# Kernel optimization log

Measured on AMD Instinct MI355X. Metric: run time of the kernel, lower is better.

## Reference

```python
import jax, jax.numpy as jnp
import numpy as np

BETA = 0.25  # cfg.vq_commitment


def setup_inputs() -> dict:
    key = jax.random.key(0)
    k1, k2 = jax.random.split(key)
    residual = jax.random.normal(k1, (16, 2048, 512), dtype=jnp.float32)
    emb_weight = jax.random.normal(k2, (1024, 512), dtype=jnp.float32) * 0.02
    return {"residual": residual, "emb_weight": emb_weight}


def reference(residual, emb_weight):
    # Euclidean branch (vq_cosine=False), no factorized projection (rvq_code_dim<=0)
    r = residual                                     # [B, T, D]
    z2 = jnp.sum(r * r, axis=-1, keepdims=True)      # [B, T, 1]
    e2 = jnp.sum(emb_weight * emb_weight, axis=-1)   # [N]
    # dist[b,t,n] = ||r_bt||^2 + ||e_n||^2 - 2 <r_bt, e_n>
    dist = z2 + e2 - 2.0 * jnp.einsum('btd,nd->btn', r, emb_weight)
    idx = jnp.argmin(dist, axis=-1)                  # [B, T] int
    z_q = emb_weight[idx]                            # gather, [B, T, D]
    # straight-through estimator
    z_st = residual + jax.lax.stop_gradient(z_q - residual)
    commit = jnp.mean((jax.lax.stop_gradient(z_q) - residual) ** 2)
    codebook = jnp.mean((z_q - jax.lax.stop_gradient(residual)) ** 2)
    loss = BETA * commit + codebook
    return (z_st, loss, dist, idx)
```

## Files before the change

### kernel.cpp

```cpp
#include <hip/hip_runtime.h>
#include <cfloat>
#include <stdint.h>

#define D       512
#define NCODES  1024
#define MROWS   32768

#define ZST_OFF  0
#define LOSS_OFF 16777216
#define DIST_OFF 16777217ull
#define IDX_OFF  50331649

#define WS_E2F   524288
#define WS_LOSSF 525312

typedef __attribute__((ext_vector_type(4))) float f32x4;
typedef __attribute__((ext_vector_type(4))) int   i32x4;
typedef __bf16 bf16v8 __attribute__((ext_vector_type(8)));

static __device__ __forceinline__ uint32_t f2bf(float x) {
    uint32_t u = __float_as_uint(x);
    return (u + 0x7fffu + ((u >> 16) & 1u)) >> 16;
}
static __device__ __forceinline__ float bf2f(uint32_t h) {
    return __uint_as_float(h << 16);
}
static __device__ __forceinline__ f32x4 MFMA(bf16v8 a, bf16v8 b, f32x4 c) {
    return __builtin_amdgcn_mfma_f32_16x16x32_bf16(a, b, c, 0, 0, 0);
}

__global__ void split_e_kernel(const float* __restrict__ emb,
                               char* __restrict__ wsb,
                               float* __restrict__ wsf) {
    if (blockIdx.x == 0 && threadIdx.x == 0) wsf[WS_LOSSF] = 0.0f;
    const int u    = blockIdx.x * 256 + threadIdx.x;
    const int row  = u >> 5;
    const int ks   = (u >> 1) & 15;
    const int half = u & 1;
    const float* p = emb + (size_t)row * D + ks * 32 + half * 16;
    float xs[16];
#pragma unroll
    for (int i = 0; i < 4; ++i) {
        const float4 v = ((const float4*)p)[i];
        xs[4*i] = v.x; xs[4*i+1] = v.y; xs[4*i+2] = v.z; xs[4*i+3] = v.w;
    }
    uint32_t hw[8], lw[8];
#pragma unroll
    for (int i = 0; i < 8; ++i) {
        const float a = xs[2*i], b = xs[2*i+1];
        const uint32_t h0 = f2bf(a), h1 = f2bf(b);
        const uint32_t l0 = f2bf(a - bf2f(h0)), l1 = f2bf(b - bf2f(h1));
        hw[i] = h0 | (h1 << 16);
        lw[i] = l0 | (l1 << 16);
    }
    const int nblk = row >> 7, col = row & 127;
    char* base = wsb + (size_t)nblk * 262144 + (size_t)ks * 16384 + col * 128;
    const int sw = col & 7;
    *(i32x4*)(base + 16 * ((half*2    ) ^ sw)) = i32x4{(int)hw[0],(int)hw[1],(int)hw[2],(int)hw[3]};
    *(i32x4*)(base + 16 * ((half*2 + 1) ^ sw)) = i32x4{(int)hw[4],(int)hw[5],(int)hw[6],(int)hw[7]};
    *(i32x4*)(base + 16 * ((4 + half*2    ) ^ sw)) = i32x4{(int)lw[0],(int)lw[1],(int)lw[2],(int)lw[3]};
    *(i32x4*)(base + 16 * ((4 + half*2 + 1) ^ sw)) = i32x4{(int)lw[4],(int)lw[5],(int)lw[6],(int)lw[7]};
}

__global__ void e2_kernel(const float* __restrict__ emb,
                          float* __restrict__ wsf) {
    const int gw   = (int)((blockIdx.x * blockDim.x + threadIdx.x) >> 6);
    const int lane = threadIdx.x & 63;
    const float4* v = (const float4*)(emb + (size_t)gw * D);
    const float4 a = v[lane * 2];
    const float4 b = v[lane * 2 + 1];
    float s = a.x*a.x + a.y*a.y + a.z*a.z + a.w*a.w
            + b.x*b.x + b.y*b.y + b.z*b.z + b.w*b.w;
#pragma unroll
    for (int off = 32; off > 0; off >>= 1) s += __shfl_xor(s, off);
    if (lane == 0) wsf[WS_E2F + gw] = s;
}

__launch_bounds__(256, 2)
__global__ void gemm_kernel(const float* __restrict__ residual,
                            const char* __restrict__ wsb,
                            const float* __restrict__ wsf,
                            float* __restrict__ out) {
    __shared__ __align__(16) char smem[66048];
    float* z2s = (float*)(smem + 65536);

    const int t    = threadIdx.x;
    const int lane = t & 63, wid = t >> 6;
    const int ln15 = lane & 15, kg = lane >> 4;
    const int wm   = wid >> 1, wn = wid & 1;

    const int bid  = blockIdx.x;
    const int xcd  = bid & 7, j = bid >> 3;
    const int mblk = xcd * 32 + (j >> 3);
    const int nblk = j & 7;
    const int row0 = mblk * 128;
    const int n0   = nblk * 128;

    const int arow = t >> 1, ahalf = t & 1;
    const float* asrc = residual + (size_t)(row0 + arow) * D + ahalf * 16;
    const int asw = arow & 7;
    char* awbase = nullptr;

    int aoffh[4], aoffl[4], boffh[4], boffl[4];
#pragma unroll
    for (int mf = 0; mf < 4; ++mf) {
        const int rA = wm * 64 + mf * 16 + ln15;
        aoffh[mf] = rA * 128 + 16 * ((    kg) ^ (rA & 7));
        aoffl[mf] = rA * 128 + 16 * ((4 + kg) ^ (rA & 7));
    }
#pragma unroll
    for (int nf = 0; nf < 4; ++nf) {
        const int cB = wn * 64 + nf * 16 + ln15;
        boffh[nf] = 16384 + cB * 128 + 16 * ((    kg) ^ (cB & 7));
        boffl[nf] = 16384 + cB * 128 + 16 * ((4 + kg) ^ (cB & 7));
    }

    const char* Bimg = wsb + (size_t)nblk * 262144;

    float z2p = 0.0f;

    auto LOAD_A = [&](int s, f32x4 na[4]) {
        const float* p = asrc + s * 32;
#pragma unroll
        for (int i = 0; i < 4; ++i) na[i] = *(const f32x4*)(p + 4 * i);
    };
    auto WRITE_A = [&](char* buf, const f32x4 na[4]) {
        float xs[16];
#pragma unroll
        for (int i = 0; i < 4; ++i) {
            xs[4*i] = na[i][0]; xs[4*i+1] = na[i][1];
            xs[4*i+2] = na[i][2]; xs[4*i+3] = na[i][3];
        }
        uint32_t hw[8], lw[8];
#pragma unroll
        for (int i = 0; i < 8; ++i) {
            const float a = xs[2*i], b = xs[2*i+1];
            z2p += a * a + b * b;
            const uint32_t h0 = f2bf(a), h1 = f2bf(b);
            const uint32_t l0 = f2bf(a - bf2f(h0)), l1 = f2bf(b - bf2f(h1));
            hw[i] = h0 | (h1 << 16);
            lw[i] = l0 | (l1 << 16);
        }
        char* base = buf + arow * 128;
        *(i32x4*)(base + 16 * ((ahalf*2    ) ^ asw)) = i32x4{(int)hw[0],(int)hw[1],(int)hw[2],(int)hw[3]};
        *(i32x4*)(base + 16 * ((ahalf*2 + 1) ^ asw)) = i32x4{(int)hw[4],(int)hw[5],(int)hw[6],(int)hw[7]};
        *(i32x4*)(base + 16 * ((4 + ahalf*2    ) ^ asw)) = i32x4{(int)lw[0],(int)lw[1],(int)lw[2],(int)lw[3]};
        *(i32x4*)(base + 16 * ((4 + ahalf*2 + 1) ^ asw)) = i32x4{(int)lw[4],(int)lw[5],(int)lw[6],(int)lw[7]};
    };
    auto STAGE_B = [&](int s, char* buf) {
        const char* gb = Bimg + (size_t)s * 16384 + wid * 4096 + lane * 16;
        char* lb = buf + 16384 + wid * 4096;
#pragma unroll
        for (int i = 0; i < 4; ++i)
            __builtin_amdgcn_global_load_lds((const uint32_t*)(gb + i * 1024),
                                             (uint32_t*)(lb + i * 1024), 16, 0, 0);
    };

    f32x4 acc[4][4];
#pragma unroll
    for (int mf = 0; mf < 4; ++mf)
#pragma unroll
        for (int nf = 0; nf < 4; ++nf) acc[mf][nf] = 0.f;

    {
        f32x4 na[4];
        LOAD_A(0, na);
        STAGE_B(0, smem);
        WRITE_A(smem, na);
    }

    for (int s = 0; s < 16; ++s) {
        __syncthreads();
        char* nbuf = smem + ((s + 1) & 1) * 32768;
        f32x4 na[4];
        if (s < 15) {
            LOAD_A(s + 1, na);
            STAGE_B(s + 1, nbuf);
        }
        const char* buf = smem + (s & 1) * 32768;

        bf16v8 ah[4], al[4], bh[4], bl[4];
#pragma unroll
        for (int mf = 0; mf < 4; ++mf) {
            ah[mf] = *(const bf16v8*)(buf + aoffh[mf]);
            al[mf] = *(const bf16v8*)(buf + aoffl[mf]);
        }
#pragma unroll
        for (int nf = 0; nf < 4; ++nf) {
            bh[nf] = *(const bf16v8*)(buf + boffh[nf]);
            bl[nf] = *(const bf16v8*)(buf + boffl[nf]);
        }
#pragma unroll
        for (int mf = 0; mf < 4; ++mf)
#pragma unroll
            for (int nf = 0; nf < 4; ++nf) {
                acc[mf][nf] = MFMA(ah[mf], bh[nf], acc[mf][nf]);
                acc[mf][nf] = MFMA(ah[mf], bl[nf], acc[mf][nf]);
                acc[mf][nf] = MFMA(al[mf], bh[nf], acc[mf][nf]);
            }

        if (s < 15) WRITE_A(nbuf, na);
    }

    __syncthreads();
    {
        const float o = __shfl_xor(z2p, 1);
        if (ahalf == 0) z2s[arow] = z2p + o;
    }
    __syncthreads();

    float e2v[4];
#pragma unroll
    for (int nf = 0; nf < 4; ++nf)
        e2v[nf] = wsf[WS_E2F + n0 + wn * 64 + nf * 16 + ln15];
#pragma unroll
    for (int mf = 0; mf < 4; ++mf)
#pragma unroll
        for (int j4 = 0; j4 < 4; ++j4) {
            const int rl = wm * 64 + mf * 16 + kg * 4 + j4;
            const float z2 = z2s[rl];
            const size_t rbase = DIST_OFF + (size_t)(row0 + rl) * 1024;
#pragma unroll
            for (int nf = 0; nf < 4; ++nf) {
                const int gcol = n0 + wn * 64 + nf * 16 + ln15;
                out[rbase + gcol] = (z2 + e2v[nf]) - 2.0f * acc[mf][nf][j4];
            }
        }
}

__global__ void argzst_kernel(const float* __restrict__ residual,
                              const float* __restrict__ emb,
                              float* __restrict__ wsf,
                              float* __restrict__ out) {
    __shared__ int   srow[64];
    __shared__ float swsum[4];
    const int t = threadIdx.x, lane = t & 63, w = t >> 6;
    const int row0 = blockIdx.x * 64;

    for (int rr = 0; rr < 16; ++rr) {
        const int row = row0 + w * 16 + rr;
        const float* dr = out + DIST_OFF + (size_t)row * 1024;
        float lv = FLT_MAX; int li = 0;
#pragma unroll
        for (int c = 0; c < 16; ++c) {
            const int col = c * 64 + lane;
            const float v = dr[col];
            if (v < lv) { lv = v; li = col; }
        }
#pragma unroll
        for (int off = 32; off > 0; off >>= 1) {
            const float ov = __shfl_xor(lv, off);
            const int   oi = __shfl_xor(li, off);
            if (ov < lv || (ov == lv && oi < li)) { lv = ov; li = oi; }
        }
        if (lane == 0) {
            srow[w * 16 + rr] = li;
            out[IDX_OFF + row] = (float)li;
        }
    }
    __syncthreads();

    float lsum = 0.0f;
    for (int e4 = t; e4 < 64 * 128; e4 += 256) {
        const int rl = e4 >> 7, dq = e4 & 127;
        const size_t gi = (size_t)(row0 + rl) * D + dq * 4;
        const float4 rv = *(const float4*)&residual[gi];
        const int code = srow[rl];
        const float4 ev = *(const float4*)&emb[(size_t)code * D + dq * 4];
        float4 st;
        const float dx = ev.x - rv.x, dy = ev.y - rv.y;
        const float dz = ev.z - rv.z, dw = ev.w - rv.w;
        st.x = rv.x + dx; st.y = rv.y + dy; st.z = rv.z + dz; st.w = rv.w + dw;
        *(float4*)&out[ZST_OFF + gi] = st;
        lsum += dx * dx + dy * dy + dz * dz + dw * dw;
    }
#pragma unroll
    for (int off = 32; off > 0; off >>= 1) lsum += __shfl_xor(lsum, off);
    if (lane == 0) swsum[w] = lsum;
    __syncthreads();
    if (t == 0) {
        float s = 0.0f;
#pragma unroll
        for (int ww = 0; ww < 4; ++ww) s += swsum[ww];
        atomicAdd(&wsf[WS_LOSSF], s);
    }
}

__global__ void finalize_kernel(const float* __restrict__ wsf,
                                float* __restrict__ out) {
    out[LOSS_OFF] = 1.25f * wsf[WS_LOSSF] / 16777216.0f;
}

extern "C" void kernel_launch(void* const* d_in, const int* in_sizes, int n_in,
                              void* d_out, int out_size, void* d_ws, size_t ws_size,
                              hipStream_t stream) {
    const float* residual = (const float*)d_in[0];
    const float* emb      = (const float*)d_in[1];
    float* out = (float*)d_out;
    char*  wsb = (char*)d_ws;
    float* wsf = (float*)d_ws;

    split_e_kernel<<<128, 256, 0, stream>>>(emb, wsb, wsf);
    e2_kernel<<<256, 256, 0, stream>>>(emb, wsf);
    gemm_kernel<<<2048, 256, 0, stream>>>(residual, wsb, wsf, out);
    argzst_kernel<<<512, 256, 0, stream>>>(residual, emb, wsf, out);
    finalize_kernel<<<1, 1, 0, stream>>>(wsf, out);
}
```

Measured before the change: 407.6 us.

## Fuse partial argmin into GEMM epilogue and single-buffer A to raise occupancy

```diff
diff --git a/kernel.cpp b/kernel.cpp
--- a/kernel.cpp
+++ b/kernel.cpp
@@ -12,7 +12,8 @@
 #define IDX_OFF  50331649
 
 #define WS_E2F   524288
-#define WS_LOSSF 525312
+#define WS_Z2F   (WS_E2F + 1024)
+#define WS_LOSSF (WS_Z2F + MROWS)
 
 typedef __attribute__((ext_vector_type(4))) float f32x4;
 typedef __attribute__((ext_vector_type(4))) int   i32x4;
@@ -62,27 +63,34 @@
     *(i32x4*)(base + 16 * ((4 + half*2 + 1) ^ sw)) = i32x4{(int)lw[4],(int)lw[5],(int)lw[6],(int)lw[7]};
 }
 
-__global__ void e2_kernel(const float* __restrict__ emb,
-                          float* __restrict__ wsf) {
+__global__ void norms_kernel(const float* __restrict__ residual,
+                             const float* __restrict__ emb,
+                             float* __restrict__ wsf) {
     const int gw   = (int)((blockIdx.x * blockDim.x + threadIdx.x) >> 6);
     const int lane = threadIdx.x & 63;
-    const float4* v = (const float4*)(emb + (size_t)gw * D);
+    const bool isR = gw < MROWS;
+    const float* src = isR ? residual + (size_t)gw * D
+                           : emb + (size_t)(gw - MROWS) * D;
+    const float4* v = (const float4*)src;
     const float4 a = v[lane * 2];
     const float4 b = v[lane * 2 + 1];
     float s = a.x*a.x + a.y*a.y + a.z*a.z + a.w*a.w
             + b.x*b.x + b.y*b.y + b.z*b.z + b.w*b.w;
 #pragma unroll
     for (int off = 32; off > 0; off >>= 1) s += __shfl_xor(s, off);
-    if (lane == 0) wsf[WS_E2F + gw] = s;
-}
-
-__launch_bounds__(256, 2)
+    if (lane == 0) {
+        if (isR) wsf[WS_Z2F + gw] = s;
+        else     wsf[WS_E2F + (gw - MROWS)] = s;
+    }
+}
+
+__launch_bounds__(256, 3)
 __global__ void gemm_kernel(const float* __restrict__ residual,
                             const char* __restrict__ wsb,
                             const float* __restrict__ wsf,
                             float* __restrict__ out) {
-    __shared__ __align__(16) char smem[66048];
-    float* z2s = (float*)(smem + 65536);
+    __shared__ __align__(16) char smem[49664];
+    float* z2s = (float*)(smem + 49152);
 
     const int t    = threadIdx.x;
     const int lane = t & 63, wid = t >> 6;
@@ -96,10 +104,12 @@
     const int row0 = mblk * 128;
     const int n0   = nblk * 128;
 
-    const int arow = t >> 1, ahalf = t & 1;
-    const float* asrc = residual + (size_t)(row0 + arow) * D + ahalf * 16;
-    const int asw = arow & 7;
-    char* awbase = nullptr;
+    const int arb  = t >> 3;
+    const int u    = (t & 7) ^ (arb & 7);
+    const int comp = u >> 2, kq = u & 3;
+    const float* aptr = residual + (size_t)(row0 + arb) * D + kq * 8;
+
+    if (t < 128) z2s[t] = wsf[WS_Z2F + row0 + t];
 
     int aoffh[4], aoffl[4], boffh[4], boffl[4];
 #pragma unroll
@@ -111,49 +121,51 @@
 #pragma unroll
     for (int nf = 0; nf < 4; ++nf) {
         const int cB = wn * 64 + nf * 16 + ln15;
-        boffh[nf] = 16384 + cB * 128 + 16 * ((    kg) ^ (cB & 7));
-        boffl[nf] = 16384 + cB * 128 + 16 * ((4 + kg) ^ (cB & 7));
+        boffh[nf] = cB * 128 + 16 * ((    kg) ^ (cB & 7));
+        boffl[nf] = cB * 128 + 16 * ((4 + kg) ^ (cB & 7));
     }
 
     const char* Bimg = wsb + (size_t)nblk * 262144;
 
-    float z2p = 0.0f;
-
-    auto LOAD_A = [&](int s, f32x4 na[4]) {
-        const float* p = asrc + s * 32;
-#pragma unroll
-        for (int i = 0; i < 4; ++i) na[i] = *(const f32x4*)(p + 4 * i);
+    float4 a0[4], a1[4];
+    auto LOAD_A = [&](int s) {
+#pragma unroll
+        for (int i = 0; i < 4; ++i) {
+            const float* p = aptr + (size_t)i * (32 * D) + s * 32;
+            a0[i] = *(const float4*)p;
+            a1[i] = *(const float4*)(p + 4);
+        }
     };
-    auto WRITE_A = [&](char* buf, const f32x4 na[4]) {
-        float xs[16];
+    auto WRITE_A = [&]() {
 #pragma unroll
         for (int i = 0; i < 4; ++i) {
-            xs[4*i] = na[i][0]; xs[4*i+1] = na[i][1];
-            xs[4*i+2] = na[i][2]; xs[4*i+3] = na[i][3];
-        }
-        uint32_t hw[8], lw[8];
-#pragma unroll
-        for (int i = 0; i < 8; ++i) {
-            const float a = xs[2*i], b = xs[2*i+1];
-            z2p += a * a + b * b;
-            const uint32_t h0 = f2bf(a), h1 = f2bf(b);
-            const uint32_t l0 = f2bf(a - bf2f(h0)), l1 = f2bf(b - bf2f(h1));
-            hw[i] = h0 | (h1 << 16);
-            lw[i] = l0 | (l1 << 16);
-        }
-        char* base = buf + arow * 128;
-        *(i32x4*)(base + 16 * ((ahalf*2    ) ^ asw)) = i32x4{(int)hw[0],(int)hw[1],(int)hw[2],(int)hw[3]};
-        *(i32x4*)(base + 16 * ((ahalf*2 + 1) ^ asw)) = i32x4{(int)hw[4],(int)hw[5],(int)hw[6],(int)hw[7]};
-        *(i32x4*)(base + 16 * ((4 + ahalf*2    ) ^ asw)) = i32x4{(int)lw[0],(int)lw[1],(int)lw[2],(int)lw[3]};
-        *(i32x4*)(base + 16 * ((4 + ahalf*2 + 1) ^ asw)) = i32x4{(int)lw[4],(int)lw[5],(int)lw[6],(int)lw[7]};
+            const float e[8] = {a0[i].x, a0[i].y, a0[i].z, a0[i].w,
+                                a1[i].x, a1[i].y, a1[i].z, a1[i].w};
+            uint32_t w[4];
+#pragma unroll
+            for (int jj = 0; jj < 4; ++jj) {
+                const uint32_t h0 = f2bf(e[2*jj]), h1 = f2bf(e[2*jj+1]);
+                uint32_t r;
+                if (comp == 0) {
+                    r = h0 | (h1 << 16);
+                } else {
+                    const uint32_t l0 = f2bf(e[2*jj]   - bf2f(h0));
+                    const uint32_t l1 = f2bf(e[2*jj+1] - bf2f(h1));
+                    r = l0 | (l1 << 16);
+                }
+                w[jj] = r;
+            }
+            *(i32x4*)(smem + i * 4096 + t * 16) =
+                i32x4{(int)w[0], (int)w[1], (int)w[2], (int)w[3]};
+        }
     };
-    auto STAGE_B = [&](int s, char* buf) {
-        const char* gb = Bimg + (size_t)s * 16384 + wid * 4096 + lane * 16;
-        char* lb = buf + 16384 + wid * 4096;
+    auto STAGE_B = [&](int s) {
+        const char* gb = Bimg + (size_t)s * 16384 + t * 16;
+        char* lb = smem + 16384 + (s & 1) * 16384 + t * 16;
 #pragma unroll
         for (int i = 0; i < 4; ++i)
-            __builtin_amdgcn_global_load_lds((const uint32_t*)(gb + i * 1024),
-                                             (uint32_t*)(lb + i * 1024), 16, 0, 0);
+            __builtin_amdgcn_global_load_lds((const uint32_t*)(gb + i * 4096),
+                                             (uint32_t*)(lb + i * 4096), 16, 0, 0);
     };
 
     f32x4 acc[4][4];
@@ -162,33 +174,26 @@
 #pragma unroll
         for (int nf = 0; nf < 4; ++nf) acc[mf][nf] = 0.f;
 
-    {
-        f32x4 na[4];
-        LOAD_A(0, na);
-        STAGE_B(0, smem);
-        WRITE_A(smem, na);
-    }
+    LOAD_A(0);
+    STAGE_B(0);
 
     for (int s = 0; s < 16; ++s) {
         __syncthreads();
-        char* nbuf = smem + ((s + 1) & 1) * 32768;
-        f32x4 na[4];
-        if (s < 15) {
-            LOAD_A(s + 1, na);
-            STAGE_B(s + 1, nbuf);
-        }
-        const char* buf = smem + (s & 1) * 32768;
-
+        WRITE_A();
+        __syncthreads();
+        if (s < 15) { LOAD_A(s + 1); STAGE_B(s + 1); }
+
+        const char* bbuf = smem + 16384 + (s & 1) * 16384;
         bf16v8 ah[4], al[4], bh[4], bl[4];
 #pragma unroll
         for (int mf = 0; mf < 4; ++mf) {
-            ah[mf] = *(const bf16v8*)(buf + aoffh[mf]);
-            al[mf] = *(const bf16v8*)(buf + aoffl[mf]);
+            ah[mf] = *(const bf16v8*)(smem + aoffh[mf]);
+            al[mf] = *(const bf16v8*)(smem + aoffl[mf]);
         }
 #pragma unroll
         for (int nf = 0; nf < 4; ++nf) {
-            bh[nf] = *(const bf16v8*)(buf + boffh[nf]);
-            bl[nf] = *(const bf16v8*)(buf + boffl[nf]);
+            bh[nf] = *(const bf16v8*)(bbuf + boffh[nf]);
+            bl[nf] = *(const bf16v8*)(bbuf + boffl[nf]);
         }
 #pragma unroll
         for (int mf = 0; mf < 4; ++mf)
@@ -198,16 +203,7 @@
                 acc[mf][nf] = MFMA(ah[mf], bl[nf], acc[mf][nf]);
                 acc[mf][nf] = MFMA(al[mf], bh[nf], acc[mf][nf]);
             }
-
-        if (s < 15) WRITE_A(nbuf, na);
-    }
-
-    __syncthreads();
-    {
-        const float o = __shfl_xor(z2p, 1);
-        if (ahalf == 0) z2s[arow] = z2p + o;
-    }
-    __syncthreads();
+    }
 
     float e2v[4];
 #pragma unroll
@@ -220,10 +216,24 @@
             const int rl = wm * 64 + mf * 16 + kg * 4 + j4;
             const float z2 = z2s[rl];
             const size_t rbase = DIST_OFF + (size_t)(row0 + rl) * 1024;
+            float bv = FLT_MAX; int bi = 0;
 #pragma unroll
             for (int nf = 0; nf < 4; ++nf) {
                 const int gcol = n0 + wn * 64 + nf * 16 + ln15;
-                out[rbase + gcol] = (z2 + e2v[nf]) - 2.0f * acc[mf][nf][j4];
+                const float dv = (z2 + e2v[nf]) - 2.0f * acc[mf][nf][j4];
+                out[rbase + gcol] = dv;
+                if (dv < bv) { bv = dv; bi = gcol; }
+            }
+#pragma unroll
+            for (int off = 1; off < 16; off <<= 1) {
+                const float ov = __shfl_xor(bv, off);
+                const int   oi = __shfl_xor(bi, off);
+                if (ov < bv || (ov == bv && oi < bi)) { bv = ov; bi = oi; }
+            }
+            if (ln15 == 0) {
+                float2 pr; pr.x = bv; pr.y = (float)bi;
+                *(float2*)&out[ZST_OFF + (size_t)(row0 + rl) * D
+                               + (nblk * 2 + wn) * 2] = pr;
             }
         }
 }
@@ -237,25 +247,23 @@
     const int t = threadIdx.x, lane = t & 63, w = t >> 6;
     const int row0 = blockIdx.x * 64;
 
-    for (int rr = 0; rr < 16; ++rr) {
-        const int row = row0 + w * 16 + rr;
-        const float* dr = out + DIST_OFF + (size_t)row * 1024;
-        float lv = FLT_MAX; int li = 0;
-#pragma unroll
-        for (int c = 0; c < 16; ++c) {
-            const int col = c * 64 + lane;
-            const float v = dr[col];
-            if (v < lv) { lv = v; li = col; }
-        }
-#pragma unroll
-        for (int off = 32; off > 0; off >>= 1) {
-            const float ov = __shfl_xor(lv, off);
-            const int   oi = __shfl_xor(li, off);
-            if (ov < lv || (ov == lv && oi < li)) { lv = ov; li = oi; }
-        }
-        if (lane == 0) {
-            srow[w * 16 + rr] = li;
-            out[IDX_OFF + row] = (float)li;
+    const int rsub = lane >> 4;
+    const int slot = lane & 15;
+#pragma unroll
+    for (int g = 0; g < 4; ++g) {
+        const int rl  = w * 16 + g * 4 + rsub;
+        const int row = row0 + rl;
+        const float2 p = *(const float2*)&out[ZST_OFF + (size_t)row * D + slot * 2];
+        float bv = p.x; float bif = p.y;
+#pragma unroll
+        for (int off = 1; off < 16; off <<= 1) {
+            const float ov  = __shfl_xor(bv, off);
+            const float oif = __shfl_xor(bif, off);
+            if (ov < bv || (ov == bv && oif < bif)) { bv = ov; bif = oif; }
+        }
+        if (slot == 0) {
+            srow[rl] = (int)bif;
+            out[IDX_OFF + row] = bif;
         }
     }
     __syncthreads();
@@ -301,7 +309,7 @@
     float* wsf = (float*)d_ws;
 
     split_e_kernel<<<128, 256, 0, stream>>>(emb, wsb, wsf);
-    e2_kernel<<<256, 256, 0, stream>>>(emb, wsf);
+    norms_kernel<<<(MROWS + NCODES) / 4, 256, 0, stream>>>(residual, emb, wsf);
     gemm_kernel<<<2048, 256, 0, stream>>>(residual, wsb, wsf, out);
     argzst_kernel<<<512, 256, 0, stream>>>(residual, emb, wsf, out);
     finalize_kernel<<<1, 1, 0, stream>>>(wsf, out);
```

Measured after the change: 386.6 us. -5.2%, faster.

## Pre-split residual into bf16 hi/lo image and fuse argmin into GEMM epilogue

Applied to the files above, without the earlier changes.

```diff
diff --git a/kernel.cpp b/kernel.cpp
--- a/kernel.cpp
+++ b/kernel.cpp
@@ -11,8 +11,10 @@
 #define DIST_OFF 16777217ull
 #define IDX_OFF  50331649
 
-#define WS_E2F   524288
-#define WS_LOSSF 525312
+#define WS_AMIN_B 2097152
+#define WS_E2F    589824
+#define WS_Z2F    590848
+#define WS_LOSSF  656384
 
 typedef __attribute__((ext_vector_type(4))) float f32x4;
 typedef __attribute__((ext_vector_type(4))) int   i32x4;
@@ -62,6 +64,48 @@
     *(i32x4*)(base + 16 * ((4 + half*2 + 1) ^ sw)) = i32x4{(int)lw[4],(int)lw[5],(int)lw[6],(int)lw[7]};
 }
 
+__global__ void split_a_kernel(const float* __restrict__ residual,
+                               float* __restrict__ wsf,
+                               float* __restrict__ out) {
+    const int mblk = blockIdx.x >> 1;
+    const int kh   = blockIdx.x & 1;
+    const int t    = threadIdx.x;
+    const int row  = t >> 1, half = t & 1;
+    const int row0 = mblk * 128;
+    const float* src = residual + (size_t)(row0 + row) * D + half * 16;
+    char* img = (char*)out + (size_t)mblk * 262144 + row * 128;
+    const int sw = row & 7;
+    float s = 0.f;
+#pragma unroll
+    for (int k8 = 0; k8 < 8; ++k8) {
+        const int ks = kh * 8 + k8;
+        const float* p = src + ks * 32;
+        float xs[16];
+#pragma unroll
+        for (int i = 0; i < 4; ++i) {
+            const float4 v = ((const float4*)p)[i];
+            xs[4*i] = v.x; xs[4*i+1] = v.y; xs[4*i+2] = v.z; xs[4*i+3] = v.w;
+        }
+        uint32_t hw[8], lw[8];
+#pragma unroll
+        for (int i = 0; i < 8; ++i) {
+            const float a = xs[2*i], b = xs[2*i+1];
+            s += a * a + b * b;
+            const uint32_t h0 = f2bf(a), h1 = f2bf(b);
+            const uint32_t l0 = f2bf(a - bf2f(h0)), l1 = f2bf(b - bf2f(h1));
+            hw[i] = h0 | (h1 << 16);
+            lw[i] = l0 | (l1 << 16);
+        }
+        char* b = img + (size_t)ks * 16384;
+        *(i32x4*)(b + 16 * ((half*2    ) ^ sw)) = i32x4{(int)hw[0],(int)hw[1],(int)hw[2],(int)hw[3]};
+        *(i32x4*)(b + 16 * ((half*2 + 1) ^ sw)) = i32x4{(int)hw[4],(int)hw[5],(int)hw[6],(int)hw[7]};
+        *(i32x4*)(b + 16 * ((4 + half*2    ) ^ sw)) = i32x4{(int)lw[0],(int)lw[1],(int)lw[2],(int)lw[3]};
+        *(i32x4*)(b + 16 * ((4 + half*2 + 1) ^ sw)) = i32x4{(int)lw[4],(int)lw[5],(int)lw[6],(int)lw[7]};
+    }
+    s += __shfl_xor(s, 1);
+    if (half == 0) wsf[WS_Z2F + (row0 + row) * 2 + kh] = s;
+}
+
 __global__ void e2_kernel(const float* __restrict__ emb,
                           float* __restrict__ wsf) {
     const int gw   = (int)((blockIdx.x * blockDim.x + threadIdx.x) >> 6);
@@ -77,9 +121,9 @@
 }
 
 __launch_bounds__(256, 2)
-__global__ void gemm_kernel(const float* __restrict__ residual,
-                            const char* __restrict__ wsb,
+__global__ void gemm_kernel(const char* __restrict__ wsb,
                             const float* __restrict__ wsf,
+                            unsigned long long* __restrict__ amin,
                             float* __restrict__ out) {
     __shared__ __align__(16) char smem[66048];
     float* z2s = (float*)(smem + 65536);
@@ -96,10 +140,8 @@
     const int row0 = mblk * 128;
     const int n0   = nblk * 128;
 
-    const int arow = t >> 1, ahalf = t & 1;
-    const float* asrc = residual + (size_t)(row0 + arow) * D + ahalf * 16;
-    const int asw = arow & 7;
-    char* awbase = nullptr;
+    if (t < 128)
+        z2s[t] = wsf[WS_Z2F + (row0 + t) * 2] + wsf[WS_Z2F + (row0 + t) * 2 + 1];
 
     int aoffh[4], aoffl[4], boffh[4], boffl[4];
 #pragma unroll
@@ -111,50 +153,28 @@
 #pragma unroll
     for (int nf = 0; nf < 4; ++nf) {
         const int cB = wn * 64 + nf * 16 + ln15;
-        boffh[nf] = 16384 + cB * 128 + 16 * ((    kg) ^ (cB & 7));
-        boffl[nf] = 16384 + cB * 128 + 16 * ((4 + kg) ^ (cB & 7));
-    }
-
+        boffh[nf] = cB * 128 + 16 * ((    kg) ^ (cB & 7));
+        boffl[nf] = cB * 128 + 16 * ((4 + kg) ^ (cB & 7));
+    }
+
+    const char* Aimg = (const char*)out + (size_t)mblk * 262144;
     const char* Bimg = wsb + (size_t)nblk * 262144;
 
-    float z2p = 0.0f;
-
-    auto LOAD_A = [&](int s, f32x4 na[4]) {
-        const float* p = asrc + s * 32;
-#pragma unroll
-        for (int i = 0; i < 4; ++i) na[i] = *(const f32x4*)(p + 4 * i);
+    auto STAGE = [&](int s) {
+        const int b = s & 1;
+        const char* ga = Aimg + (size_t)s * 16384 + t * 16;
+        char* la = smem + b * 16384 + t * 16;
+#pragma unroll
+        for (int i = 0; i < 4; ++i)
+            __builtin_amdgcn_global_load_lds((const uint32_t*)(ga + i * 4096),
+                                             (uint32_t*)(la + i * 4096), 16, 0, 0);
+        const char* gb = Bimg + (size_t)s * 16384 + t * 16;
+        char* lb = smem + 32768 + b * 16384 + t * 16;
+#pragma unroll
+        for (int i = 0; i < 4; ++i)
+            __builtin_amdgcn_global_load_lds((const uint32_t*)(gb + i * 4096),
+                                             (uint32_t*)(lb + i * 4096), 16, 0, 0);
     };
-    auto WRITE_A = [&](char* buf, const f32x4 na[4]) {
-        float xs[16];
-#pragma unroll
-        for (int i = 0; i < 4; ++i) {
-            xs[4*i] = na[i][0]; xs[4*i+1] = na[i][1];
-            xs[4*i+2] = na[i][2]; xs[4*i+3] = na[i][3];
-        }
-        uint32_t hw[8], lw[8];
-#pragma unroll
-        for (int i = 0; i < 8; ++i) {
-            const float a = xs[2*i], b = xs[2*i+1];
-            z2p += a * a + b * b;
-            const uint32_t h0 = f2bf(a), h1 = f2bf(b);
-            const uint32_t l0 = f2bf(a - bf2f(h0)), l1 = f2bf(b - bf2f(h1));
-            hw[i] = h0 | (h1 << 16);
-            lw[i] = l0 | (l1 << 16);
-        }
-        char* base = buf + arow * 128;
-        *(i32x4*)(base + 16 * ((ahalf*2    ) ^ asw)) = i32x4{(int)hw[0],(int)hw[1],(int)hw[2],(int)hw[3]};
-        *(i32x4*)(base + 16 * ((ahalf*2 + 1) ^ asw)) = i32x4{(int)hw[4],(int)hw[5],(int)hw[6],(int)hw[7]};
-        *(i32x4*)(base + 16 * ((4 + ahalf*2    ) ^ asw)) = i32x4{(int)lw[0],(int)lw[1],(int)lw[2],(int)lw[3]};
-        *(i32x4*)(base + 16 * ((4 + ahalf*2 + 1) ^ asw)) = i32x4{(int)lw[4],(int)lw[5],(int)lw[6],(int)lw[7]};
-    };
-    auto STAGE_B = [&](int s, char* buf) {
-        const char* gb = Bimg + (size_t)s * 16384 + wid * 4096 + lane * 16;
-        char* lb = buf + 16384 + wid * 4096;
-#pragma unroll
-        for (int i = 0; i < 4; ++i)
-            __builtin_amdgcn_global_load_lds((const uint32_t*)(gb + i * 1024),
-                                             (uint32_t*)(lb + i * 1024), 16, 0, 0);
-    };
 
     f32x4 acc[4][4];
 #pragma unroll
@@ -162,33 +182,24 @@
 #pragma unroll
         for (int nf = 0; nf < 4; ++nf) acc[mf][nf] = 0.f;
 
-    {
-        f32x4 na[4];
-        LOAD_A(0, na);
-        STAGE_B(0, smem);
-        WRITE_A(smem, na);
-    }
+    STAGE(0);
 
     for (int s = 0; s < 16; ++s) {
         __syncthreads();
-        char* nbuf = smem + ((s + 1) & 1) * 32768;
-        f32x4 na[4];
-        if (s < 15) {
-            LOAD_A(s + 1, na);
-            STAGE_B(s + 1, nbuf);
-        }
-        const char* buf = smem + (s & 1) * 32768;
-
+        if (s < 15) STAGE(s + 1);
+
+        const char* abuf = smem + (s & 1) * 16384;
+        const char* bbuf = smem + 32768 + (s & 1) * 16384;
         bf16v8 ah[4], al[4], bh[4], bl[4];
 #pragma unroll
         for (int mf = 0; mf < 4; ++mf) {
-            ah[mf] = *(const bf16v8*)(buf + aoffh[mf]);
-            al[mf] = *(const bf16v8*)(buf + aoffl[mf]);
+            ah[mf] = *(const bf16v8*)(abuf + aoffh[mf]);
+            al[mf] = *(const bf16v8*)(abuf + aoffl[mf]);
         }
 #pragma unroll
         for (int nf = 0; nf < 4; ++nf) {
-            bh[nf] = *(const bf16v8*)(buf + boffh[nf]);
-            bl[nf] = *(const bf16v8*)(buf + boffl[nf]);
+            bh[nf] = *(const bf16v8*)(bbuf + boffh[nf]);
+            bl[nf] = *(const bf16v8*)(bbuf + boffl[nf]);
         }
 #pragma unroll
         for (int mf = 0; mf < 4; ++mf)
@@ -198,16 +209,7 @@
                 acc[mf][nf] = MFMA(ah[mf], bl[nf], acc[mf][nf]);
                 acc[mf][nf] = MFMA(al[mf], bh[nf], acc[mf][nf]);
             }
-
-        if (s < 15) WRITE_A(nbuf, na);
-    }
-
-    __syncthreads();
-    {
-        const float o = __shfl_xor(z2p, 1);
-        if (ahalf == 0) z2s[arow] = z2p + o;
-    }
-    __syncthreads();
+    }
 
     float e2v[4];
 #pragma unroll
@@ -220,16 +222,33 @@
             const int rl = wm * 64 + mf * 16 + kg * 4 + j4;
             const float z2 = z2s[rl];
             const size_t rbase = DIST_OFF + (size_t)(row0 + rl) * 1024;
+            float bv = FLT_MAX; int bi = 0;
 #pragma unroll
             for (int nf = 0; nf < 4; ++nf) {
                 const int gcol = n0 + wn * 64 + nf * 16 + ln15;
-                out[rbase + gcol] = (z2 + e2v[nf]) - 2.0f * acc[mf][nf][j4];
+                const float dv = (z2 + e2v[nf]) - 2.0f * acc[mf][nf][j4];
+                out[rbase + gcol] = dv;
+                if (dv < bv) { bv = dv; bi = gcol; }
+            }
+#pragma unroll
+            for (int off = 1; off < 16; off <<= 1) {
+                const float ov = __shfl_xor(bv, off);
+                const int   oi = __shfl_xor(bi, off);
+                if (ov < bv || (ov == bv && oi < bi)) { bv = ov; bi = oi; }
+            }
+            if (ln15 == 0) {
+                const uint32_t u   = __float_as_uint(bv);
+                const uint32_t key = u ^ ((uint32_t)((int)u >> 31) | 0x80000000u);
+                const unsigned long long pk =
+                    ((unsigned long long)key << 32) | (uint32_t)bi;
+                atomicMin(&amin[row0 + rl], pk);
             }
         }
 }
 
 __global__ void argzst_kernel(const float* __restrict__ residual,
                               const float* __restrict__ emb,
+                              const unsigned long long* __restrict__ amin,
                               float* __restrict__ wsf,
                               float* __restrict__ out) {
     __shared__ int   srow[64];
@@ -237,26 +256,11 @@
     const int t = threadIdx.x, lane = t & 63, w = t >> 6;
     const int row0 = blockIdx.x * 64;
 
-    for (int rr = 0; rr < 16; ++rr) {
-        const int row = row0 + w * 16 + rr;
-        const float* dr = out + DIST_OFF + (size_t)row * 1024;
-        float lv = FLT_MAX; int li = 0;
-#pragma unroll
-        for (int c = 0; c < 16; ++c) {
-            const int col = c * 64 + lane;
-            const float v = dr[col];
-            if (v < lv) { lv = v; li = col; }
-        }
-#pragma unroll
-        for (int off = 32; off > 0; off >>= 1) {
-            const float ov = __shfl_xor(lv, off);
-            const int   oi = __shfl_xor(li, off);
-            if (ov < lv || (ov == lv && oi < li)) { lv = ov; li = oi; }
-        }
-        if (lane == 0) {
-            srow[w * 16 + rr] = li;
-            out[IDX_OFF + row] = (float)li;
-        }
+    if (t < 64) {
+        const unsigned long long p = amin[row0 + t];
+        const int idx = (int)(p & 0xFFFFFFFFull);
+        srow[t] = idx;
+        out[IDX_OFF + row0 + t] = (float)idx;
     }
     __syncthreads();
 
@@ -299,10 +303,14 @@
     float* out = (float*)d_out;
     char*  wsb = (char*)d_ws;
     float* wsf = (float*)d_ws;
-
+    unsigned long long* amin =
+        (unsigned long long*)((char*)d_ws + WS_AMIN_B);
+
+    hipMemsetAsync((char*)d_ws + WS_AMIN_B, 0xFF, 262144, stream);
     split_e_kernel<<<128, 256, 0, stream>>>(emb, wsb, wsf);
+    split_a_kernel<<<512, 256, 0, stream>>>(residual, wsf, out);
     e2_kernel<<<256, 256, 0, stream>>>(emb, wsf);
-    gemm_kernel<<<2048, 256, 0, stream>>>(residual, wsb, wsf, out);
-    argzst_kernel<<<512, 256, 0, stream>>>(residual, emb, wsf, out);
+    gemm_kernel<<<2048, 256, 0, stream>>>(wsb, wsf, amin, out);
+    argzst_kernel<<<512, 256, 0, stream>>>(residual, emb, amin, wsf, out);
     finalize_kernel<<<1, 1, 0, stream>>>(wsf, out);
 }
```

Result: no change. 414.7 us (+1.7%).
